# Performance work log

Measured on AMD Instinct MI355X. Metric: run time of the kernel, lower is better.

## Reference

```python
import jax, jax.numpy as jnp
import numpy as np

NUM_CODES = 8192
DIM = 8
BETA = 0.25
TAU = 1.0
EPS = 1e-10


def setup_inputs() -> dict:
    key = jax.random.key(0)
    k1, k2, k3 = jax.random.split(key, 3)
    z_e = jax.random.normal(k1, (8, DIM, 32, 32), dtype=jnp.float32)
    embedding = jax.random.normal(k2, (NUM_CODES, DIM), dtype=jnp.float32) * 0.01
    proj_w = jax.random.normal(k3, (NUM_CODES, DIM), dtype=jnp.float32) * (1.0 / np.sqrt(DIM))
    return {"z_e": z_e, "embedding": embedding, "proj_w": proj_w}


def reference(z_e, embedding, proj_w):
    B, D, H, W = z_e.shape
    K = embedding.shape[0]
    # (B, D, H, W) -> (N, D), N = B*H*W  (matches permute(0,2,3,1).reshape(-1,d))
    z_flat = jnp.transpose(z_e, (0, 2, 3, 1)).reshape(-1, D)
    # 1x1 conv == matmul against (K, D) weight
    logits = z_flat @ proj_w.T  # (N, K)  -- dominant memory traffic
    # Gumbel-softmax with hard=True (training path), fixed noise key
    u = jax.random.uniform(jax.random.key(42), logits.shape,
                           dtype=logits.dtype, minval=1e-20, maxval=1.0)
    gumbel = -jnp.log(-jnp.log(u))
    y_soft = jax.nn.softmax((logits + gumbel) / TAU, axis=-1)
    idx = jnp.argmax(y_soft, axis=-1)  # (N,)
    y_hard = jax.nn.one_hot(idx, K, dtype=y_soft.dtype)
    # straight-through: forward = hard one-hot, backward = soft
    st = y_hard + y_soft - jax.lax.stop_gradient(y_soft)
    z_q_flat = st @ embedding  # (N, D) -- effectively a gather in forward
    z_q = jnp.transpose(z_q_flat.reshape(B, H, W, D), (0, 3, 1, 2))
    # commitment loss against detached re-lookup
    q_flat = jax.lax.stop_gradient(embedding[idx])
    commit_loss = BETA * jnp.mean((z_flat - q_flat) ** 2)
    # usage stats (no-grad in original)
    counts = jnp.zeros((K,), z_e.dtype).at[idx].add(1.0)
    avg = counts / idx.shape[0]
    perplexity = jnp.exp(-jnp.sum(avg * jnp.log(avg + EPS)))
    usage = jnp.sum(counts > 0).astype(z_e.dtype) / K
    indices = idx.reshape(B, H, W)
    return z_q, indices, commit_loss, perplexity, usage
```

## Files before the change

kernel.cpp:

```cpp
#include <hip/hip_runtime.h>
#include <stdint.h>


#define NCODES 8192
#define NROWS  8192
#define NBLOCKS 2048

__device__ int   g_hist[NCODES];
__device__ int   g_done;
__device__ float g_commit;


#define TF4_R1T \
  "v_alignbit_b32 %0, %4, %4, 19\n" "v_alignbit_b32 %1, %5, %5, 19\n" \
  "v_alignbit_b32 %2, %6, %6, 19\n" "v_alignbit_b32 %3, %7, %7, 19\n" \
  "v_xor_b32 %0, %0, %4\n" "v_xor_b32 %1, %1, %5\n" \
  "v_xor_b32 %2, %2, %6\n" "v_xor_b32 %3, %3, %7\n"

#define TF4_ADD \
  "v_add_u32 %4, %4, %0\n" "v_add_u32 %5, %5, %1\n" \
  "v_add_u32 %6, %6, %2\n" "v_add_u32 %7, %7, %3\n"

#define TF4_ADD3_42 \
  "v_add3_u32 %4, %4, %0, 42\n" "v_add3_u32 %5, %5, %1, 42\n" \
  "v_add3_u32 %6, %6, %2, 42\n" "v_add3_u32 %7, %7, %3, 42\n"

#define TF4_ROT(s) \
  "v_alignbit_b32 %0, %0, %0, " #s "\n" "v_alignbit_b32 %1, %1, %1, " #s "\n" \
  "v_alignbit_b32 %2, %2, %2, " #s "\n" "v_alignbit_b32 %3, %3, %3, " #s "\n"

#define TF4_XOR \
  "v_xor_b32 %0, %0, %4\n" "v_xor_b32 %1, %1, %5\n" \
  "v_xor_b32 %2, %2, %6\n" "v_xor_b32 %3, %3, %7\n"

#define TF4_AX1(lit) \
  "v_add_u32 %0, " #lit ", %0\n" "v_add_u32 %1, " #lit ", %1\n" \
  "v_add_u32 %2, " #lit ", %2\n" "v_add_u32 %3, " #lit ", %3\n"

#define TF4_AX0(lit) \
  "v_add_u32 %4, " #lit ", %4\n" "v_add_u32 %5, " #lit ", %5\n" \
  "v_add_u32 %6, " #lit ", %6\n" "v_add_u32 %7, " #lit ", %7\n"

#define TF4_RN(s)  TF4_ADD     TF4_ROT(s) TF4_XOR
#define TF4_RN3(s) TF4_ADD3_42 TF4_ROT(s) TF4_XOR

#define GVQ_C   0.36651292058166435f
#define GVQ_LN2 0.69314718055994530942f
__device__ __forceinline__ float gvq20_gumbel(uint32_t bits) {
    float u = __uint_as_float(__builtin_amdgcn_alignbit(0x7Fu, bits, 9u)) - 1.0f;
    float l1 = __builtin_amdgcn_logf(u);
    float l2 = __builtin_amdgcn_logf(-l1);
    return fmaf(-GVQ_LN2, l2, GVQ_C);
}

#define DOT8(zz) \
    fmaf(zz[7], wb.w, fmaf(zz[6], wb.z, fmaf(zz[5], wb.y, fmaf(zz[4], wb.x, \
    fmaf(zz[3], wa.w, fmaf(zz[2], wa.z, fmaf(zz[1], wa.y, zz[0] * wa.x)))))))

__global__ __launch_bounds__(256, 6) void gvq20_argmax(const float* __restrict__ z_e,
                                                       const float* __restrict__ proj_w,
                                                       const float* __restrict__ emb,
                                                       float* __restrict__ out) {
    __shared__ float sv[4][256];
    __shared__ int   sj[4][256];
    __shared__ float ssq[4];
    __shared__ int   is_last;
    const int tid = threadIdx.x;
    const int n0 = blockIdx.x * 4;

    float z0[8], z1[8], z2[8], z3[8];
#pragma unroll
    for (int d = 0; d < 8; ++d) {
        const int nA = n0 + 0, nB = n0 + 1, nC = n0 + 2, nD = n0 + 3;
        z0[d] = z_e[(nA >> 10) * 8192 + d * 1024 + (nA & 1023)];
        z1[d] = z_e[(nB >> 10) * 8192 + d * 1024 + (nB & 1023)];
        z2[d] = z_e[(nC >> 10) * 8192 + d * 1024 + (nC & 1023)];
        z3[d] = z_e[(nD >> 10) * 8192 + d * 1024 + (nD & 1023)];
    }

    const uint32_t ba = ((uint32_t)(n0 + 0) << 13) + (uint32_t)tid + 42u;
    const uint32_t bb = ((uint32_t)(n0 + 1) << 13) + (uint32_t)tid + 42u;
    const uint32_t bc = ((uint32_t)(n0 + 2) << 13) + (uint32_t)tid + 42u;
    const uint32_t bd = ((uint32_t)(n0 + 3) << 13) + (uint32_t)tid + 42u;

    const float4* p = ((const float4*)proj_w) + 2 * tid;
    float best0 = -INFINITY, best1 = -INFINITY, best2 = -INFINITY, best3 = -INFINITY;
    int bi0 = 0, bi1 = 0, bi2 = 0, bi3 = 0;

    for (int i = 0; i < 32; ++i) {
        float4 wa = p[0];
        float4 wb = p[1];
        p += 512;

        float d0 = DOT8(z0);
        float d1 = DOT8(z1);
        float d2 = DOT8(z2);
        float d3 = DOT8(z3);

        const uint32_t soff = (uint32_t)(i << 8);
        uint32_t xa = ba + soff, xb = bb + soff, xc = bc + soff, xd = bd + soff;
        uint32_t o0, o1, o2, o3;
        asm(TF4_R1T
            TF4_RN(17) TF4_RN(6) TF4_RN(26)
            TF4_AX1(0x1BD11BF1)
            TF4_RN3(15) TF4_RN(3) TF4_RN(16) TF4_RN(8)
            TF4_AX0(0x1BD11BF0) TF4_AX1(2)
            TF4_RN(19) TF4_RN(17) TF4_RN(6) TF4_RN(26)
            TF4_AX1(45)
            TF4_RN(15) TF4_RN(3) TF4_RN(16) TF4_RN(8)
            TF4_AX1(0x1BD11BF4)
            TF4_RN3(19) TF4_RN(17) TF4_RN(6) TF4_RN(26)
            TF4_AX0(0x1BD11BF0) TF4_AX1(5)
            TF4_XOR
            : "=&v"(o0), "=&v"(o1), "=&v"(o2), "=&v"(o3),
              "+v"(xa), "+v"(xb), "+v"(xc), "+v"(xd));

        float v0 = d0 + gvq20_gumbel(o0);
        float v1 = d1 + gvq20_gumbel(o1);
        float v2 = d2 + gvq20_gumbel(o2);
        float v3 = d3 + gvq20_gumbel(o3);

        if (v0 > best0) { best0 = v0; bi0 = i; }
        if (v1 > best1) { best1 = v1; bi1 = i; }
        if (v2 > best2) { best2 = v2; bi2 = i; }
        if (v3 > best3) { best3 = v3; bi3 = i; }
    }

    sv[0][tid] = best0; sj[0][tid] = (bi0 << 8) + tid;
    sv[1][tid] = best1; sj[1][tid] = (bi1 << 8) + tid;
    sv[2][tid] = best2; sj[2][tid] = (bi2 << 8) + tid;
    sv[3][tid] = best3; sj[3][tid] = (bi3 << 8) + tid;
    __syncthreads();
    for (int s = 128; s > 0; s >>= 1) {
        if (tid < s) {
#pragma unroll
            for (int r = 0; r < 4; ++r) {
                float va = sv[r][tid + s];
                int   ja = sj[r][tid + s];
                if (va > sv[r][tid] || (va == sv[r][tid] && ja < sj[r][tid])) {
                    sv[r][tid] = va; sj[r][tid] = ja;
                }
            }
        }
        __syncthreads();
    }

    if (tid < 4) {
        const int n = n0 + tid;
        const int idx = sj[tid][0];
        out[65536 + n] = (float)idx;
        atomicAdd(&g_hist[idx], 1);
        float zz[8];
#pragma unroll
        for (int d = 0; d < 8; ++d) {
            zz[d] = (tid == 0) ? z0[d] : (tid == 1) ? z1[d]
                  : (tid == 2) ? z2[d] : z3[d];
        }
        const float4* ep = (const float4*)(emb + idx * 8);
        float4 ea = ep[0], eb = ep[1];
        float e[8] = {ea.x, ea.y, ea.z, ea.w, eb.x, eb.y, eb.z, eb.w};
        const int b = n >> 10, r = n & 1023;
        float sq = 0.0f;
#pragma unroll
        for (int d = 0; d < 8; ++d) {
            out[b * 8192 + d * 1024 + r] = e[d];
            float diff = zz[d] - e[d];
            sq = fmaf(diff, diff, sq);
        }
        ssq[tid] = sq;
    }
    __syncthreads();
    if (tid == 0) {
        atomicAdd(&g_commit, ssq[0] + ssq[1] + ssq[2] + ssq[3]);
        asm volatile("s_waitcnt vmcnt(0)" ::: "memory");
        int old = __hip_atomic_fetch_add(&g_done, 1, __ATOMIC_RELAXED,
                                         __HIP_MEMORY_SCOPE_AGENT);
        is_last = (old == NBLOCKS - 1);
    }
    __syncthreads();

    if (is_last) {
        float h = 0.0f; int used = 0;
        for (int kk = tid; kk < NCODES; kk += 256) {
            int c = __hip_atomic_load(&g_hist[kk], __ATOMIC_RELAXED,
                                      __HIP_MEMORY_SCOPE_AGENT);
            float avg = (float)c * (1.0f / 8192.0f);
            h += avg * logf(avg + 1e-10f);
            used += (c > 0) ? 1 : 0;
            g_hist[kk] = 0;
        }
        sv[0][tid] = h; sj[0][tid] = used;
        __syncthreads();
        for (int s = 128; s > 0; s >>= 1) {
            if (tid < s) { sv[0][tid] += sv[0][tid + s]; sj[0][tid] += sj[0][tid + s]; }
            __syncthreads();
        }
        if (tid == 0) {
            float accum = __hip_atomic_load(&g_commit, __ATOMIC_RELAXED,
                                            __HIP_MEMORY_SCOPE_AGENT);
            out[73728] = 0.25f * accum * (1.0f / 65536.0f);
            out[73729] = expf(-sv[0][0]);
            out[73730] = (float)sj[0][0] * (1.0f / 8192.0f);
            g_commit = 0.0f;
            g_done = 0;
        }
    }
}

extern "C" void kernel_launch(void* const* d_in, const int* in_sizes, int n_in,
                              void* d_out, int out_size, void* d_ws, size_t ws_size,
                              hipStream_t stream) {
    const float* z_e   = (const float*)d_in[0];
    const float* emb   = (const float*)d_in[1];
    const float* projw = (const float*)d_in[2];
    float* out = (float*)d_out;

    gvq20_argmax<<<NBLOCKS, 256, 0, stream>>>(z_e, projw, emb, out);
}
```

Measured before the change: 227.6 us.

## Split last-block finalize into separate init and stats kernels

```diff
diff --git a/kernel.cpp b/kernel.cpp
--- a/kernel.cpp
+++ b/kernel.cpp
@@ -6,9 +6,7 @@
 #define NROWS  8192
 #define NBLOCKS 2048
 
-__device__ int   g_hist[NCODES];
-__device__ int   g_done;
-__device__ float g_commit;
+__device__ int g_hist[NCODES];
 
 
 #define TF4_R1T \
@@ -46,25 +44,30 @@
 
 #define GVQ_C   0.36651292058166435f
 #define GVQ_LN2 0.69314718055994530942f
-__device__ __forceinline__ float gvq20_gumbel(uint32_t bits) {
+__device__ __forceinline__ float gvq21_gumbel(uint32_t bits) {
     float u = __uint_as_float(__builtin_amdgcn_alignbit(0x7Fu, bits, 9u)) - 1.0f;
     float l1 = __builtin_amdgcn_logf(u);
     float l2 = __builtin_amdgcn_logf(-l1);
     return fmaf(-GVQ_LN2, l2, GVQ_C);
 }
 
+__global__ __launch_bounds__(1024) void gvq21_init(float* out) {
+    const int t = threadIdx.x;
+    for (int k = t; k < NCODES; k += 1024) g_hist[k] = 0;
+    if (t == 0) out[73728] = 0.0f;
+}
+
 #define DOT8(zz) \
     fmaf(zz[7], wb.w, fmaf(zz[6], wb.z, fmaf(zz[5], wb.y, fmaf(zz[4], wb.x, \
     fmaf(zz[3], wa.w, fmaf(zz[2], wa.z, fmaf(zz[1], wa.y, zz[0] * wa.x)))))))
 
-__global__ __launch_bounds__(256, 6) void gvq20_argmax(const float* __restrict__ z_e,
+__global__ __launch_bounds__(256, 5) void gvq21_argmax(const float* __restrict__ z_e,
                                                        const float* __restrict__ proj_w,
                                                        const float* __restrict__ emb,
                                                        float* __restrict__ out) {
     __shared__ float sv[4][256];
     __shared__ int   sj[4][256];
     __shared__ float ssq[4];
-    __shared__ int   is_last;
     const int tid = threadIdx.x;
     const int n0 = blockIdx.x * 4;
 
@@ -115,10 +118,10 @@
             : "=&v"(o0), "=&v"(o1), "=&v"(o2), "=&v"(o3),
               "+v"(xa), "+v"(xb), "+v"(xc), "+v"(xd));
 
-        float v0 = d0 + gvq20_gumbel(o0);
-        float v1 = d1 + gvq20_gumbel(o1);
-        float v2 = d2 + gvq20_gumbel(o2);
-        float v3 = d3 + gvq20_gumbel(o3);
+        float v0 = d0 + gvq21_gumbel(o0);
+        float v1 = d1 + gvq21_gumbel(o1);
+        float v2 = d2 + gvq21_gumbel(o2);
+        float v3 = d3 + gvq21_gumbel(o3);
 
         if (v0 > best0) { best0 = v0; bi0 = i; }
         if (v1 > best1) { best1 = v1; bi1 = i; }
@@ -170,40 +173,33 @@
         ssq[tid] = sq;
     }
     __syncthreads();
+    if (tid == 0)
+        atomicAdd(out + 73728, ssq[0] + ssq[1] + ssq[2] + ssq[3]);
+}
+
+__global__ __launch_bounds__(1024) void gvq21_stats(float* __restrict__ out) {
+    __shared__ float hred[1024];
+    __shared__ int   ired[1024];
+    const int tid = threadIdx.x;
+
+    float h = 0.0f; int used = 0;
+    for (int kk = tid; kk < NCODES; kk += 1024) {
+        int c = g_hist[kk];
+        float avg = (float)c * (1.0f / 8192.0f);
+        h += avg * logf(avg + 1e-10f);
+        used += (c > 0) ? 1 : 0;
+    }
+    hred[tid] = h; ired[tid] = used;
+    __syncthreads();
+    for (int t = 512; t > 0; t >>= 1) {
+        if (tid < t) { hred[tid] += hred[tid + t]; ired[tid] += ired[tid + t]; }
+        __syncthreads();
+    }
     if (tid == 0) {
-        atomicAdd(&g_commit, ssq[0] + ssq[1] + ssq[2] + ssq[3]);
-        asm volatile("s_waitcnt vmcnt(0)" ::: "memory");
-        int old = __hip_atomic_fetch_add(&g_done, 1, __ATOMIC_RELAXED,
-                                         __HIP_MEMORY_SCOPE_AGENT);
-        is_last = (old == NBLOCKS - 1);
-    }
-    __syncthreads();
-
-    if (is_last) {
-        float h = 0.0f; int used = 0;
-        for (int kk = tid; kk < NCODES; kk += 256) {
-            int c = __hip_atomic_load(&g_hist[kk], __ATOMIC_RELAXED,
-                                      __HIP_MEMORY_SCOPE_AGENT);
-            float avg = (float)c * (1.0f / 8192.0f);
-            h += avg * logf(avg + 1e-10f);
-            used += (c > 0) ? 1 : 0;
-            g_hist[kk] = 0;
-        }
-        sv[0][tid] = h; sj[0][tid] = used;
-        __syncthreads();
-        for (int s = 128; s > 0; s >>= 1) {
-            if (tid < s) { sv[0][tid] += sv[0][tid + s]; sj[0][tid] += sj[0][tid + s]; }
-            __syncthreads();
-        }
-        if (tid == 0) {
-            float accum = __hip_atomic_load(&g_commit, __ATOMIC_RELAXED,
-                                            __HIP_MEMORY_SCOPE_AGENT);
-            out[73728] = 0.25f * accum * (1.0f / 65536.0f);
-            out[73729] = expf(-sv[0][0]);
-            out[73730] = (float)sj[0][0] * (1.0f / 8192.0f);
-            g_commit = 0.0f;
-            g_done = 0;
-        }
+        float accum = out[73728];
+        out[73728] = 0.25f * accum * (1.0f / 65536.0f);
+        out[73729] = expf(-hred[0]);
+        out[73730] = (float)ired[0] * (1.0f / 8192.0f);
     }
 }
 
@@ -215,5 +211,7 @@
     const float* projw = (const float*)d_in[2];
     float* out = (float*)d_out;
 
-    gvq20_argmax<<<NBLOCKS, 256, 0, stream>>>(z_e, projw, emb, out);
-}
+    gvq21_init  <<<1,       1024, 0, stream>>>(out);
+    gvq21_argmax<<<NBLOCKS, 256,  0, stream>>>(z_e, projw, emb, out);
+    gvq21_stats <<<1,       1024, 0, stream>>>(out);
+}
```

Result: faster. 212.4 us (-6.7%).
